# Kernel tuning notes

Hardware: AMD Instinct MI355X
Metric: run time of the kernel (lower is better)

The kernel has to match this reference:

```python
import math
import jax, jax.numpy as jnp
import numpy as np

B, L, D_M, H, D_K, D_V = 2, 2048, 1024, 16, 64, 64


def setup_inputs() -> dict:
    key = jax.random.key(0)
    ks = jax.random.split(key, 12)
    s_in = 1.0 / math.sqrt(D_M)
    s_cat = 1.0 / math.sqrt(H * D_V)
    return {
        "Q": jax.random.normal(ks[0], (B, L, D_M), jnp.float32),
        "K": jax.random.normal(ks[1], (B, L, D_M), jnp.float32),
        "V": jax.random.normal(ks[2], (B, L, D_M), jnp.float32),
        # per-head projections batched along a leading head axis
        "Wq": jax.random.uniform(ks[3], (H, D_M, D_K), jnp.float32, -s_in, s_in),
        "bq": jax.random.uniform(ks[4], (H, D_K), jnp.float32, -s_in, s_in),
        "Wk": jax.random.uniform(ks[5], (H, D_M, D_K), jnp.float32, -s_in, s_in),
        "bk": jax.random.uniform(ks[6], (H, D_K), jnp.float32, -s_in, s_in),
        "Wv": jax.random.uniform(ks[7], (H, D_M, D_V), jnp.float32, -s_in, s_in),
        "bv": jax.random.uniform(ks[8], (H, D_V), jnp.float32, -s_in, s_in),
        "Wo": jax.random.uniform(ks[9], (H * D_V, D_M), jnp.float32, -s_cat, s_cat),
        "bo": jax.random.uniform(ks[10], (D_M,), jnp.float32, -s_cat, s_cat),
    }


def reference(Q, K, V, Wq, bq, Wk, bk, Wv, bv, Wo, bo):
    # Batched per-head projections: [B,L,Dm] x [H,Dm,Dk] -> [B,H,L,Dk]
    Qp = jnp.einsum("bqm,hmk->bhqk", Q, Wq) + bq[None, :, None, :]
    Kp = jnp.einsum("bsm,hmk->bhsk", K, Wk) + bk[None, :, None, :]
    Vp = jnp.einsum("bsm,hmv->bhsv", V, Wv) + bv[None, :, None, :]
    scores = jnp.einsum("bhqk,bhsk->bhqs", Qp, Kp) / jnp.sqrt(
        jnp.asarray(D_K, Qp.dtype)
    )
    # NOTE: original torch code uses Softmax(dim=1) on a [B,Lq,Lk] matrix,
    # i.e. normalization over the QUERY axis (axis=2 here), not the key axis.
    attn = jax.nn.softmax(scores, axis=2)
    wV = jnp.einsum("bhqs,bhsv->bhqv", attn, Vp)  # [B,H,Lq,Dv]
    cat_V = jnp.transpose(wV, (0, 2, 1, 3)).reshape(B, L, H * D_V)
    return cat_V @ Wo + bo
```

## Files before the change

### kernel.cpp

```cpp
#include <hip/hip_runtime.h>
#include <hip/hip_bf16.h>

#define DEVI __device__ __forceinline__

typedef __hip_bfloat16 bf16;
typedef __attribute__((ext_vector_type(8))) __bf16 bf16x8;
typedef __attribute__((ext_vector_type(4))) float f32x4;
typedef __attribute__((ext_vector_type(4))) short short4v;
typedef __attribute__((ext_vector_type(8))) short short8v;


DEVI short bfbits(float f) { bf16 h = __float2bfloat16(f); return *(short*)&h; }
DEVI float b2f(short s) { union { float f; unsigned u; } c; c.u = ((unsigned)(unsigned short)s) << 16; return c.f; }

DEVI void gl16(const void* g, void* l) {
  __builtin_amdgcn_global_load_lds((const __attribute__((address_space(1))) void*)g,
                                   (__attribute__((address_space(3))) void*)l, 16, 0, 0);
}

DEVI f32x4 MF(bf16x8 a, bf16x8 b, f32x4 c) {
  return __builtin_amdgcn_mfma_f32_16x16x32_bf16(a, b, c, 0, 0, 0);
}

DEVI int swzE(int row, int ec) { return row * 64 + (ec ^ ((row & 7) << 3)); }
DEVI int srcC(int boff) { return (boff & 127) ^ (((boff >> 7) & 7) << 4); }

__global__ __launch_bounds__(256) void k_cvt_qkv(
    const float* __restrict__ Q, const float* __restrict__ K, const float* __restrict__ V,
    bf16* __restrict__ Qb, bf16* __restrict__ Kb, bf16* __restrict__ Vb) {
  const float* s = blockIdx.y == 0 ? Q : (blockIdx.y == 1 ? K : V);
  bf16* d = blockIdx.y == 0 ? Qb : (blockIdx.y == 1 ? Kb : Vb);
  int i = (blockIdx.x * 256 + threadIdx.x) * 4;
  float4 v = *(const float4*)(s + i);
  short4v o;
  o[0] = bfbits(v.x); o[1] = bfbits(v.y); o[2] = bfbits(v.z); o[3] = bfbits(v.w);
  *(short4v*)(d + i) = o;
}

__global__ __launch_bounds__(256) void k_prep_w(
    const float* __restrict__ Wq, const float* __restrict__ Wk, const float* __restrict__ Wv,
    const float* __restrict__ Wo,
    bf16* __restrict__ WqT, bf16* __restrict__ WkT, bf16* __restrict__ WvT,
    bf16* __restrict__ WoT) {
  __shared__ float t[64][65];
  const int z = blockIdx.z;
  const float* in; bf16* out; int ldin, ldout;
  if (z < 3) {
    const float* W = z == 0 ? Wq : (z == 1 ? Wk : Wv);
    bf16* O = z == 0 ? WqT : (z == 1 ? WkT : WvT);
    const int hh = blockIdx.y, m0 = blockIdx.x * 64;
    in = W + hh * 65536 + m0 * 64; ldin = 64;
    out = O + hh * 65536 + m0;     ldout = 1024;
  } else {
    const int r0 = blockIdx.x * 64, c0 = blockIdx.y * 64;
    in = Wo + r0 * 1024 + c0; ldin = 1024;
    out = WoT + c0 * 1024 + r0; ldout = 1024;
  }
  const int tx = threadIdx.x & 63, ty = threadIdx.x >> 6;
  for (int r = ty; r < 64; r += 4) t[r][tx] = in[r * ldin + tx];
  __syncthreads();
  for (int c = ty; c < 64; c += 4) out[c * ldout + tx] = __float2bfloat16(t[tx][c]);
}

__global__ __launch_bounds__(256) void k_proj_gemm(
    const bf16* __restrict__ Qb, const bf16* __restrict__ Kb, const bf16* __restrict__ Vb,
    const bf16* __restrict__ WqT, const bf16* __restrict__ WkT, const bf16* __restrict__ WvT,
    const float* __restrict__ bq, const float* __restrict__ bk, const float* __restrict__ bv,
    bf16* __restrict__ Qp, bf16* __restrict__ Kp, bf16* __restrict__ VpT) {
  __shared__ bf16 smem[17408];
  bf16* As = smem;
  bf16* Bs = smem + 8192;
  const int z = blockIdx.z;
  const bf16* A  = z == 0 ? Qb : (z == 1 ? Kb : Vb);
  const bf16* BT = z == 0 ? WqT : (z == 1 ? WkT : WvT);
  const float* bias = z == 0 ? bq : (z == 1 ? bk : bv);
  const int row0 = blockIdx.x * 128, col0 = blockIdx.y * 128;
  const int tid = threadIdx.x, lane = tid & 63, wave = tid >> 6;
  const int wq = wave >> 1, wn = wave & 1;
  f32x4 acc[4][4];
#pragma unroll
  for (int i = 0; i < 4; ++i)
#pragma unroll
    for (int j = 0; j < 4; ++j) acc[i][j] = (f32x4)0.0f;

  for (int k0 = 0; k0 < 1024; k0 += 64) {
#pragma unroll
    for (int it = 0; it < 4; ++it) {
      int boff = (it * 4 + wave) * 1024 + lane * 16;
      int r = boff >> 7, c = srcC(boff);
      gl16((const char*)A  + (size_t)(row0 + r) * 2048 + k0 * 2 + c, (char*)As + boff);
      gl16((const char*)BT + (size_t)(col0 + r) * 2048 + k0 * 2 + c, (char*)Bs + boff);
    }
    __syncthreads();
#pragma unroll
    for (int ks = 0; ks < 2; ++ks) {
      bf16x8 a[4], b[4];
#pragma unroll
      for (int i = 0; i < 4; ++i)
        a[i] = *(const bf16x8*)&As[swzE(wq * 64 + i * 16 + (lane & 15), ks * 32 + (lane >> 4) * 8)];
#pragma unroll
      for (int j = 0; j < 4; ++j)
        b[j] = *(const bf16x8*)&Bs[swzE(wn * 64 + j * 16 + (lane & 15), ks * 32 + (lane >> 4) * 8)];
#pragma unroll
      for (int i = 0; i < 4; ++i)
#pragma unroll
        for (int j = 0; j < 4; ++j) acc[i][j] = MF(a[i], b[j], acc[i][j]);
    }
    __syncthreads();
  }

  if (z < 2) {
    const float scl = (z == 0) ? 0.125f : 1.0f;
    bf16* C = z == 0 ? Qp : Kp;
#pragma unroll
    for (int i = 0; i < 4; ++i)
#pragma unroll
      for (int j = 0; j < 4; ++j) {
        int col = col0 + wn * 64 + j * 16 + (lane & 15);
        float bb = bias[col];
#pragma unroll
        for (int r = 0; r < 4; ++r) {
          int row = row0 + wq * 64 + i * 16 + (lane >> 4) * 4 + r;
          C[row * 1024 + col] = __float2bfloat16((acc[i][j][r] + bb) * scl);
        }
      }
  } else {
    bf16* T = smem;
#pragma unroll
    for (int i = 0; i < 4; ++i)
#pragma unroll
      for (int j = 0; j < 4; ++j) {
        int nl = wn * 64 + j * 16 + (lane & 15);
        float bb = bias[col0 + nl];
#pragma unroll
        for (int r = 0; r < 4; ++r) {
          int sl = wq * 64 + i * 16 + (lane >> 4) * 4 + r;
          T[nl * 136 + sl] = __float2bfloat16(acc[i][j][r] + bb);
        }
      }
    __syncthreads();
    const int b = row0 >> 11, lr = row0 & 2047;
    const int nl = tid >> 1, half = tid & 1;
    const int n = col0 + nl;
    bf16* drow = VpT + ((size_t)(b * 16 + (n >> 6)) * 64 + (n & 63)) * 2048 + lr + half * 64;
#pragma unroll
    for (int k = 0; k < 8; ++k)
      *(short8v*)(drow + k * 8) = *(const short8v*)&T[nl * 136 + half * 64 + k * 8];
  }
}

__global__ __launch_bounds__(512, 4) void k_stats(
    const bf16* __restrict__ Qp, const bf16* __restrict__ Kp, bf16* __restrict__ VpT) {
  __shared__ bf16 Ks[128 * 64];
  __shared__ bf16 Qs[2][64 * 64];
  __shared__ float zs[128];
  const int id = blockIdx.x;
  const int sw = (id & 7) * 64 + (id >> 3);
  const int bh = sw >> 4, s0 = (sw & 15) * 128;
  const int b = bh >> 4, h = bh & 15;
  const char* Qrow = (const char*)(Qp + (size_t)(b * 2048) * 1024 + h * 64);
  const char* Krow = (const char*)(Kp + (size_t)(b * 2048) * 1024 + h * 64);
  const int tid = threadIdx.x, lane = tid & 63, wave = tid >> 6;

  {
    int boff = tid * 16;
#pragma unroll
    for (int it = 0; it < 2; ++it) {
      int bo = boff + it * 8192;
      gl16(Krow + (size_t)(s0 + (bo >> 7)) * 2048 + srcC(bo), (char*)Ks + bo);
    }
    gl16(Qrow + (size_t)(boff >> 7) * 2048 + srcC(boff), (char*)Qs[0] + boff);
  }
  __syncthreads();
  bf16x8 afr[2];
#pragma unroll
  for (int ks = 0; ks < 2; ++ks)
    afr[ks] = *(const bf16x8*)&Ks[swzE(wave * 16 + (lane & 15), ks * 32 + (lane >> 4) * 8)];

  float zr[4] = {0.f, 0.f, 0.f, 0.f};
  for (int c = 0; c < 32; ++c) {
    const int p = c & 1;
    if (c < 31) {
      int boff = tid * 16;
      gl16(Qrow + (size_t)((c + 1) * 64 + (boff >> 7)) * 2048 + srcC(boff), (char*)Qs[p ^ 1] + boff);
    }
    f32x4 acc[4];
#pragma unroll
    for (int qf = 0; qf < 4; ++qf) acc[qf] = (f32x4)0.0f;
#pragma unroll
    for (int ks = 0; ks < 2; ++ks) {
      bf16x8 bfr[4];
#pragma unroll
      for (int qf = 0; qf < 4; ++qf)
        bfr[qf] = *(const bf16x8*)&Qs[p][swzE(qf * 16 + (lane & 15), ks * 32 + (lane >> 4) * 8)];
#pragma unroll
      for (int qf = 0; qf < 4; ++qf) acc[qf] = MF(afr[ks], bfr[qf], acc[qf]);
    }
#pragma unroll
    for (int qf = 0; qf < 4; ++qf)
#pragma unroll
      for (int r = 0; r < 4; ++r) zr[r] += __expf(acc[qf][r]);
    __syncthreads();
  }
#pragma unroll
  for (int m = 1; m <= 8; m <<= 1)
#pragma unroll
    for (int r = 0; r < 4; ++r) zr[r] += __shfl_xor(zr[r], m);
  if ((lane & 15) == 0) {
#pragma unroll
    for (int r = 0; r < 4; ++r) zs[wave * 16 + (lane >> 4) * 4 + r] = 1.0f / zr[r];
  }
  __syncthreads();
  {
    const int v = tid >> 3, seg = tid & 7;
    bf16* base = VpT + (size_t)(bh * 64 + v) * 2048 + s0 + seg * 16;
    short8v x0 = *(const short8v*)base;
    short8v x1 = *(const short8v*)(base + 8);
    short8v o0, o1;
#pragma unroll
    for (int j = 0; j < 8; ++j) {
      o0[j] = bfbits(b2f(x0[j]) * zs[seg * 16 + j]);
      o1[j] = bfbits(b2f(x1[j]) * zs[seg * 16 + 8 + j]);
    }
    *(short8v*)base = o0;
    *(short8v*)(base + 8) = o1;
  }
}

__global__ __launch_bounds__(512, 4) void k_attn_pv(
    const bf16* __restrict__ Qp, const bf16* __restrict__ Kp, const bf16* __restrict__ VpT,
    bf16* __restrict__ wV) {
  __shared__ bf16 QPs[128 * 64];
  __shared__ bf16 Ks[2][64 * 64];
  __shared__ bf16 Vs[2][64 * 64];
  const int id = blockIdx.x;
  const int sw = (id & 7) * 64 + (id >> 3);
  const int bh = sw >> 4, q0 = (sw & 15) * 128;
  const int b = bh >> 4, h = bh & 15;
  const char* Qrow = (const char*)(Qp + (size_t)(b * 2048) * 1024 + h * 64);
  const char* Krow = (const char*)(Kp + (size_t)(b * 2048) * 1024 + h * 64);
  const char* Vrow = (const char*)(VpT + (size_t)bh * 64 * 2048);
  const int tid = threadIdx.x, lane = tid & 63, wave = tid >> 6;

  {
    int boff = tid * 16;
#pragma unroll
    for (int it = 0; it < 2; ++it) {
      int bo = boff + it * 8192;
      gl16(Qrow + (size_t)(q0 + (bo >> 7)) * 2048 + srcC(bo), (char*)QPs + bo);
    }
    gl16(Krow + (size_t)(boff >> 7) * 2048 + srcC(boff), (char*)Ks[0] + boff);
    gl16(Vrow + (size_t)(boff >> 7) * 4096 + srcC(boff), (char*)Vs[0] + boff);
  }
  __syncthreads();
  bf16x8 aq[2];
#pragma unroll
  for (int ks = 0; ks < 2; ++ks)
    aq[ks] = *(const bf16x8*)&QPs[swzE(wave * 16 + (lane & 15), ks * 32 + (lane >> 4) * 8)];

  f32x4 acco[4];
#pragma unroll
  for (int vf = 0; vf < 4; ++vf) acco[vf] = (f32x4)0.0f;

  for (int c = 0; c < 32; ++c) {
    const int p = c & 1;
    if (c < 31) {
      int boff = tid * 16;
      gl16(Krow + (size_t)((c + 1) * 64 + (boff >> 7)) * 2048 + srcC(boff), (char*)Ks[p ^ 1] + boff);
      gl16(Vrow + (size_t)(boff >> 7) * 4096 + (c + 1) * 128 + srcC(boff), (char*)Vs[p ^ 1] + boff);
    }
    f32x4 sacc[4];
#pragma unroll
    for (int sf = 0; sf < 4; ++sf) sacc[sf] = (f32x4)0.0f;
#pragma unroll
    for (int ks = 0; ks < 2; ++ks) {
      bf16x8 bk_[4];
#pragma unroll
      for (int sf = 0; sf < 4; ++sf)
        bk_[sf] = *(const bf16x8*)&Ks[p][swzE(sf * 16 + (lane & 15), ks * 32 + (lane >> 4) * 8)];
#pragma unroll
      for (int sf = 0; sf < 4; ++sf) sacc[sf] = MF(aq[ks], bk_[sf], sacc[sf]);
    }
#pragma unroll
    for (int sf = 0; sf < 4; ++sf) {
      int sl = sf * 16 + (lane & 15);
#pragma unroll
      for (int r = 0; r < 4; ++r) {
        int row = wave * 16 + (lane >> 4) * 4 + r;
        QPs[swzE(row, sl)] = __float2bfloat16(__expf(sacc[sf][r]));
      }
    }
#pragma unroll
    for (int ks = 0; ks < 2; ++ks) {
      bf16x8 pa = *(const bf16x8*)&QPs[swzE(wave * 16 + (lane & 15), ks * 32 + (lane >> 4) * 8)];
      bf16x8 pb[4];
#pragma unroll
      for (int vf = 0; vf < 4; ++vf)
        pb[vf] = *(const bf16x8*)&Vs[p][swzE(vf * 16 + (lane & 15), ks * 32 + (lane >> 4) * 8)];
#pragma unroll
      for (int vf = 0; vf < 4; ++vf) acco[vf] = MF(pa, pb[vf], acco[vf]);
    }
    __syncthreads();
  }

#pragma unroll
  for (int vf = 0; vf < 4; ++vf) {
    int v = vf * 16 + (lane & 15);
#pragma unroll
    for (int r = 0; r < 4; ++r)
      QPs[swzE(wave * 16 + (lane >> 4) * 4 + r, v)] = __float2bfloat16(acco[vf][r]);
  }
  {
    const int rr = wave * 16 + (lane >> 2);
    const int x = (rr & 7) << 3;
    short8v x0 = *(const short8v*)&QPs[rr * 64 + (((lane & 3) * 16) ^ x)];
    short8v x1 = *(const short8v*)&QPs[rr * 64 + (((lane & 3) * 16 + 8) ^ x)];
    bf16* dst = wV + ((size_t)bh * 2048 + q0 + rr) * 64 + (lane & 3) * 16;
    *(short8v*)dst = x0;
    *(short8v*)(dst + 8) = x1;
  }
}

__global__ __launch_bounds__(256) void k_out_gemm(
    const bf16* __restrict__ wV, const bf16* __restrict__ WoT, const float* __restrict__ bo,
    float* __restrict__ out) {
  __shared__ bf16 As[128 * 64], Bs[128 * 64];
  const int row0 = blockIdx.x * 128, col0 = blockIdx.y * 128;
  const int tid = threadIdx.x, lane = tid & 63, wave = tid >> 6;
  const int wq = wave >> 1, wn = wave & 1;
  const int b = row0 >> 11, lr = row0 & 2047;
  f32x4 acc[4][4];
#pragma unroll
  for (int i = 0; i < 4; ++i)
#pragma unroll
    for (int j = 0; j < 4; ++j) acc[i][j] = (f32x4)0.0f;

  for (int k0 = 0; k0 < 1024; k0 += 64) {
    const char* Abase = (const char*)(wV + ((size_t)(b * 16 + (k0 >> 6)) * 2048 + lr) * 64);
#pragma unroll
    for (int it = 0; it < 4; ++it) {
      int boff = (it * 4 + wave) * 1024 + lane * 16;
      int r = boff >> 7, c = srcC(boff);
      gl16(Abase + (size_t)r * 128 + c, (char*)As + boff);
      gl16((const char*)WoT + (size_t)(col0 + r) * 2048 + k0 * 2 + c, (char*)Bs + boff);
    }
    __syncthreads();
#pragma unroll
    for (int ks = 0; ks < 2; ++ks) {
      bf16x8 a[4], bb[4];
#pragma unroll
      for (int i = 0; i < 4; ++i)
        a[i] = *(const bf16x8*)&As[swzE(wq * 64 + i * 16 + (lane & 15), ks * 32 + (lane >> 4) * 8)];
#pragma unroll
      for (int j = 0; j < 4; ++j)
        bb[j] = *(const bf16x8*)&Bs[swzE(wn * 64 + j * 16 + (lane & 15), ks * 32 + (lane >> 4) * 8)];
#pragma unroll
      for (int i = 0; i < 4; ++i)
#pragma unroll
        for (int j = 0; j < 4; ++j) acc[i][j] = MF(a[i], bb[j], acc[i][j]);
    }
    __syncthreads();
  }
#pragma unroll
  for (int i = 0; i < 4; ++i)
#pragma unroll
    for (int j = 0; j < 4; ++j) {
      int col = col0 + wn * 64 + j * 16 + (lane & 15);
      float bb = bo[col];
#pragma unroll
      for (int r = 0; r < 4; ++r) {
        int row = row0 + wq * 64 + i * 16 + (lane >> 4) * 4 + r;
        out[row * 1024 + col] = acc[i][j][r] + bb;
      }
    }
}

extern "C" void kernel_launch(void* const* d_in, const int* in_sizes, int n_in,
                              void* d_out, int out_size, void* d_ws, size_t ws_size,
                              hipStream_t stream) {
  (void)in_sizes; (void)n_in; (void)out_size; (void)ws_size;
  const float* Q  = (const float*)d_in[0];
  const float* K  = (const float*)d_in[1];
  const float* V  = (const float*)d_in[2];
  const float* Wq = (const float*)d_in[3];
  const float* bq = (const float*)d_in[4];
  const float* Wk = (const float*)d_in[5];
  const float* bk = (const float*)d_in[6];
  const float* Wv = (const float*)d_in[7];
  const float* bv = (const float*)d_in[8];
  const float* Wo = (const float*)d_in[9];
  const float* bo = (const float*)d_in[10];

  char* ws = (char*)d_ws;
  bf16* Qb  = (bf16*)(ws);
  bf16* Kb  = (bf16*)(ws + (8u  << 20));
  bf16* Vb  = (bf16*)(ws + (16u << 20));
  bf16* WqT = (bf16*)(ws + (24u << 20));
  bf16* WkT = (bf16*)(ws + (26u << 20));
  bf16* WvT = (bf16*)(ws + (28u << 20));
  bf16* WoT = (bf16*)(ws + (30u << 20));
  bf16* Qp  = (bf16*)(ws + (32u << 20));
  bf16* Kp  = (bf16*)(ws + (40u << 20));
  bf16* VpT = (bf16*)(ws + (48u << 20));
  bf16* wVn = (bf16*)(ws + (56u << 20));

  k_cvt_qkv <<<dim3(4096, 3), 256, 0, stream>>>(Q, K, V, Qb, Kb, Vb);
  k_prep_w  <<<dim3(16, 16, 4), 256, 0, stream>>>(Wq, Wk, Wv, Wo, WqT, WkT, WvT, WoT);
  k_proj_gemm<<<dim3(32, 8, 3), 256, 0, stream>>>(Qb, Kb, Vb, WqT, WkT, WvT, bq, bk, bv, Qp, Kp, VpT);
  k_stats   <<<512, 512, 0, stream>>>(Qp, Kp, VpT);
  k_attn_pv <<<512, 512, 0, stream>>>(Qp, Kp, VpT, wVn);
  k_out_gemm<<<dim3(32, 8), 256, 0, stream>>>(wVn, WoT, bo, (float*)d_out);
}
```

Measured before the change: 262.5 us.

## Switch attention kernels to 32x32x16 MFMA with register-resident P via permlane swap

The stats and attention-PV kernels move from 16x16x32 to 32x32x16 bf16 MFMA, with 4 waves of 32 rows each instead of 8 waves of 16 rows. In k_attn_pv the exp'd score tile is packed to bf16 with v_cvt_pk and rearranged with v_permlane32_swap, so it feeds the PV MFMA straight from registers instead of round-tripping through LDS. The output is also written directly from registers. This cuts LDS traffic and the number of MFMA instructions, at the cost of more registers per thread and fewer threads per block.

```diff
diff --git a/kernel.cpp b/kernel.cpp
--- a/kernel.cpp
+++ b/kernel.cpp
@@ -6,6 +6,7 @@
 typedef __hip_bfloat16 bf16;
 typedef __attribute__((ext_vector_type(8))) __bf16 bf16x8;
 typedef __attribute__((ext_vector_type(4))) float f32x4;
+typedef __attribute__((ext_vector_type(16))) float f32x16;
 typedef __attribute__((ext_vector_type(4))) short short4v;
 typedef __attribute__((ext_vector_type(8))) short short8v;
 
@@ -20,6 +21,23 @@
 
 DEVI f32x4 MF(bf16x8 a, bf16x8 b, f32x4 c) {
   return __builtin_amdgcn_mfma_f32_16x16x32_bf16(a, b, c, 0, 0, 0);
+}
+DEVI f32x16 MF32(bf16x8 a, bf16x8 b, f32x16 c) {
+  return __builtin_amdgcn_mfma_f32_32x32x16_bf16(a, b, c, 0, 0, 0);
+}
+
+DEVI unsigned cvtpk(float lo, float hi) {
+  unsigned w;
+  asm("v_cvt_pk_bf16_f32 %0, %1, %2" : "=v"(w) : "v"(lo), "v"(hi));
+  return w;
+}
+DEVI void swap32(unsigned& a, unsigned& b) {
+  asm volatile("v_permlane32_swap_b32 %0, %1" : "+v"(a), "+v"(b));
+}
+DEVI bf16x8 packB(unsigned w0, unsigned w1, unsigned w2, unsigned w3) {
+  union { unsigned u[4]; bf16x8 v; } t;
+  t.u[0] = w0; t.u[1] = w1; t.u[2] = w2; t.u[3] = w3;
+  return t.v;
 }
 
 DEVI int swzE(int row, int ec) { return row * 64 + (ec ^ ((row & 7) << 3)); }
@@ -149,9 +167,9 @@
   }
 }
 
-__global__ __launch_bounds__(512, 4) void k_stats(
+__global__ __launch_bounds__(256, 2) void k_stats(
     const bf16* __restrict__ Qp, const bf16* __restrict__ Kp, bf16* __restrict__ VpT) {
-  __shared__ bf16 Ks[128 * 64];
+  __shared__ bf16 Kband[128 * 64];
   __shared__ bf16 Qs[2][64 * 64];
   __shared__ float zs[128];
   const int id = blockIdx.x;
@@ -160,77 +178,77 @@
   const int b = bh >> 4, h = bh & 15;
   const char* Qrow = (const char*)(Qp + (size_t)(b * 2048) * 1024 + h * 64);
   const char* Krow = (const char*)(Kp + (size_t)(b * 2048) * 1024 + h * 64);
-  const int tid = threadIdx.x, lane = tid & 63, wave = tid >> 6;
+  const int tid = threadIdx.x, lane = tid & 63, wq = tid >> 6;
+  const int ln31 = lane & 31, hf = lane >> 5;
 
   {
     int boff = tid * 16;
 #pragma unroll
-    for (int it = 0; it < 2; ++it) {
-      int bo = boff + it * 8192;
-      gl16(Krow + (size_t)(s0 + (bo >> 7)) * 2048 + srcC(bo), (char*)Ks + bo);
+    for (int it = 0; it < 4; ++it) {
+      int bo = boff + it * 4096;
+      gl16(Krow + (size_t)(s0 + (bo >> 7)) * 2048 + srcC(bo), (char*)Kband + bo);
     }
     gl16(Qrow + (size_t)(boff >> 7) * 2048 + srcC(boff), (char*)Qs[0] + boff);
+    gl16(Qrow + (size_t)((boff + 4096) >> 7) * 2048 + srcC(boff + 4096), (char*)Qs[0] + boff + 4096);
   }
   __syncthreads();
-  bf16x8 afr[2];
-#pragma unroll
-  for (int ks = 0; ks < 2; ++ks)
-    afr[ks] = *(const bf16x8*)&Ks[swzE(wave * 16 + (lane & 15), ks * 32 + (lane >> 4) * 8)];
-
-  float zr[4] = {0.f, 0.f, 0.f, 0.f};
+  bf16x8 kf[4];
+#pragma unroll
+  for (int ks = 0; ks < 4; ++ks)
+    kf[ks] = *(const bf16x8*)&Kband[swzE(wq * 32 + ln31, ks * 16 + hf * 8)];
+
+  float zp[16];
+#pragma unroll
+  for (int r = 0; r < 16; ++r) zp[r] = 0.f;
+
   for (int c = 0; c < 32; ++c) {
     const int p = c & 1;
     if (c < 31) {
       int boff = tid * 16;
       gl16(Qrow + (size_t)((c + 1) * 64 + (boff >> 7)) * 2048 + srcC(boff), (char*)Qs[p ^ 1] + boff);
-    }
-    f32x4 acc[4];
-#pragma unroll
-    for (int qf = 0; qf < 4; ++qf) acc[qf] = (f32x4)0.0f;
-#pragma unroll
-    for (int ks = 0; ks < 2; ++ks) {
-      bf16x8 bfr[4];
-#pragma unroll
-      for (int qf = 0; qf < 4; ++qf)
-        bfr[qf] = *(const bf16x8*)&Qs[p][swzE(qf * 16 + (lane & 15), ks * 32 + (lane >> 4) * 8)];
-#pragma unroll
-      for (int qf = 0; qf < 4; ++qf) acc[qf] = MF(afr[ks], bfr[qf], acc[qf]);
-    }
-#pragma unroll
-    for (int qf = 0; qf < 4; ++qf)
-#pragma unroll
-      for (int r = 0; r < 4; ++r) zr[r] += __expf(acc[qf][r]);
-    __syncthreads();
-  }
-#pragma unroll
-  for (int m = 1; m <= 8; m <<= 1)
-#pragma unroll
-    for (int r = 0; r < 4; ++r) zr[r] += __shfl_xor(zr[r], m);
-  if ((lane & 15) == 0) {
-#pragma unroll
-    for (int r = 0; r < 4; ++r) zs[wave * 16 + (lane >> 4) * 4 + r] = 1.0f / zr[r];
+      gl16(Qrow + (size_t)((c + 1) * 64 + ((boff + 4096) >> 7)) * 2048 + srcC(boff + 4096),
+           (char*)Qs[p ^ 1] + boff + 4096);
+    }
+    f32x16 sacc0 = (f32x16)0.0f, sacc1 = (f32x16)0.0f;
+#pragma unroll
+    for (int ks = 0; ks < 4; ++ks) {
+      bf16x8 qf0 = *(const bf16x8*)&Qs[p][swzE(ln31, ks * 16 + hf * 8)];
+      bf16x8 qf1 = *(const bf16x8*)&Qs[p][swzE(32 + ln31, ks * 16 + hf * 8)];
+      sacc0 = MF32(kf[ks], qf0, sacc0);
+      sacc1 = MF32(kf[ks], qf1, sacc1);
+    }
+#pragma unroll
+    for (int r = 0; r < 16; ++r) zp[r] += __expf(sacc0[r]) + __expf(sacc1[r]);
+    __syncthreads();
+  }
+#pragma unroll
+  for (int m = 1; m <= 16; m <<= 1)
+#pragma unroll
+    for (int r = 0; r < 16; ++r) zp[r] += __shfl_xor(zp[r], m);
+  if (ln31 == 0) {
+#pragma unroll
+    for (int r = 0; r < 16; ++r)
+      zs[wq * 32 + (r & 3) + 8 * (r >> 2) + 4 * hf] = 1.0f / zp[r];
   }
   __syncthreads();
   {
-    const int v = tid >> 3, seg = tid & 7;
-    bf16* base = VpT + (size_t)(bh * 64 + v) * 2048 + s0 + seg * 16;
-    short8v x0 = *(const short8v*)base;
-    short8v x1 = *(const short8v*)(base + 8);
-    short8v o0, o1;
-#pragma unroll
-    for (int j = 0; j < 8; ++j) {
-      o0[j] = bfbits(b2f(x0[j]) * zs[seg * 16 + j]);
-      o1[j] = bfbits(b2f(x1[j]) * zs[seg * 16 + 8 + j]);
-    }
-    *(short8v*)base = o0;
-    *(short8v*)(base + 8) = o1;
-  }
-}
-
-__global__ __launch_bounds__(512, 4) void k_attn_pv(
+    const int v = tid >> 2, sseg = (tid & 3) * 32;
+    bf16* base = VpT + (size_t)(bh * 64 + v) * 2048 + s0 + sseg;
+#pragma unroll
+    for (int t = 0; t < 4; ++t) {
+      short8v x = *(const short8v*)(base + t * 8);
+      short8v o;
+#pragma unroll
+      for (int j = 0; j < 8; ++j) o[j] = bfbits(b2f(x[j]) * zs[sseg + t * 8 + j]);
+      *(short8v*)(base + t * 8) = o;
+    }
+  }
+}
+
+__global__ __launch_bounds__(256, 2) void k_attn_pv(
     const bf16* __restrict__ Qp, const bf16* __restrict__ Kp, const bf16* __restrict__ VpT,
     bf16* __restrict__ wV) {
-  __shared__ bf16 QPs[128 * 64];
+  __shared__ bf16 Qs[128 * 64];
   __shared__ bf16 Ks[2][64 * 64];
   __shared__ bf16 Vs[2][64 * 64];
   const int id = blockIdx.x;
@@ -240,84 +258,91 @@
   const char* Qrow = (const char*)(Qp + (size_t)(b * 2048) * 1024 + h * 64);
   const char* Krow = (const char*)(Kp + (size_t)(b * 2048) * 1024 + h * 64);
   const char* Vrow = (const char*)(VpT + (size_t)bh * 64 * 2048);
-  const int tid = threadIdx.x, lane = tid & 63, wave = tid >> 6;
+  const int tid = threadIdx.x, lane = tid & 63, wq = tid >> 6;
+  const int ln31 = lane & 31, hf = lane >> 5;
 
   {
     int boff = tid * 16;
 #pragma unroll
+    for (int it = 0; it < 4; ++it) {
+      int bo = boff + it * 4096;
+      gl16(Qrow + (size_t)(q0 + (bo >> 7)) * 2048 + srcC(bo), (char*)Qs + bo);
+    }
+#pragma unroll
     for (int it = 0; it < 2; ++it) {
-      int bo = boff + it * 8192;
-      gl16(Qrow + (size_t)(q0 + (bo >> 7)) * 2048 + srcC(bo), (char*)QPs + bo);
-    }
-    gl16(Krow + (size_t)(boff >> 7) * 2048 + srcC(boff), (char*)Ks[0] + boff);
-    gl16(Vrow + (size_t)(boff >> 7) * 4096 + srcC(boff), (char*)Vs[0] + boff);
+      int bo = boff + it * 4096;
+      gl16(Krow + (size_t)(bo >> 7) * 2048 + srcC(bo), (char*)Ks[0] + bo);
+      gl16(Vrow + (size_t)(bo >> 7) * 4096 + srcC(bo), (char*)Vs[0] + bo);
+    }
   }
   __syncthreads();
-  bf16x8 aq[2];
-#pragma unroll
-  for (int ks = 0; ks < 2; ++ks)
-    aq[ks] = *(const bf16x8*)&QPs[swzE(wave * 16 + (lane & 15), ks * 32 + (lane >> 4) * 8)];
-
-  f32x4 acco[4];
-#pragma unroll
-  for (int vf = 0; vf < 4; ++vf) acco[vf] = (f32x4)0.0f;
+  bf16x8 qf[4];
+#pragma unroll
+  for (int ks = 0; ks < 4; ++ks)
+    qf[ks] = *(const bf16x8*)&Qs[swzE(wq * 32 + ln31, ks * 16 + hf * 8)];
+
+  f32x16 oacc0 = (f32x16)0.0f, oacc1 = (f32x16)0.0f;
 
   for (int c = 0; c < 32; ++c) {
     const int p = c & 1;
     if (c < 31) {
       int boff = tid * 16;
-      gl16(Krow + (size_t)((c + 1) * 64 + (boff >> 7)) * 2048 + srcC(boff), (char*)Ks[p ^ 1] + boff);
-      gl16(Vrow + (size_t)(boff >> 7) * 4096 + (c + 1) * 128 + srcC(boff), (char*)Vs[p ^ 1] + boff);
-    }
-    f32x4 sacc[4];
-#pragma unroll
-    for (int sf = 0; sf < 4; ++sf) sacc[sf] = (f32x4)0.0f;
-#pragma unroll
-    for (int ks = 0; ks < 2; ++ks) {
-      bf16x8 bk_[4];
-#pragma unroll
-      for (int sf = 0; sf < 4; ++sf)
-        bk_[sf] = *(const bf16x8*)&Ks[p][swzE(sf * 16 + (lane & 15), ks * 32 + (lane >> 4) * 8)];
-#pragma unroll
-      for (int sf = 0; sf < 4; ++sf) sacc[sf] = MF(aq[ks], bk_[sf], sacc[sf]);
-    }
-#pragma unroll
-    for (int sf = 0; sf < 4; ++sf) {
-      int sl = sf * 16 + (lane & 15);
-#pragma unroll
-      for (int r = 0; r < 4; ++r) {
-        int row = wave * 16 + (lane >> 4) * 4 + r;
-        QPs[swzE(row, sl)] = __float2bfloat16(__expf(sacc[sf][r]));
-      }
-    }
-#pragma unroll
-    for (int ks = 0; ks < 2; ++ks) {
-      bf16x8 pa = *(const bf16x8*)&QPs[swzE(wave * 16 + (lane & 15), ks * 32 + (lane >> 4) * 8)];
-      bf16x8 pb[4];
-#pragma unroll
-      for (int vf = 0; vf < 4; ++vf)
-        pb[vf] = *(const bf16x8*)&Vs[p][swzE(vf * 16 + (lane & 15), ks * 32 + (lane >> 4) * 8)];
-#pragma unroll
-      for (int vf = 0; vf < 4; ++vf) acco[vf] = MF(pa, pb[vf], acco[vf]);
-    }
-    __syncthreads();
-  }
-
-#pragma unroll
-  for (int vf = 0; vf < 4; ++vf) {
-    int v = vf * 16 + (lane & 15);
-#pragma unroll
-    for (int r = 0; r < 4; ++r)
-      QPs[swzE(wave * 16 + (lane >> 4) * 4 + r, v)] = __float2bfloat16(acco[vf][r]);
-  }
+#pragma unroll
+      for (int it = 0; it < 2; ++it) {
+        int bo = boff + it * 4096;
+        gl16(Krow + (size_t)((c + 1) * 64 + (bo >> 7)) * 2048 + srcC(bo), (char*)Ks[p ^ 1] + bo);
+        gl16(Vrow + (size_t)(bo >> 7) * 4096 + (c + 1) * 128 + srcC(bo), (char*)Vs[p ^ 1] + bo);
+      }
+    }
+    f32x16 sacc0 = (f32x16)0.0f, sacc1 = (f32x16)0.0f;
+#pragma unroll
+    for (int ks = 0; ks < 4; ++ks) {
+      bf16x8 kf0 = *(const bf16x8*)&Ks[p][swzE(ln31, ks * 16 + hf * 8)];
+      bf16x8 kf1 = *(const bf16x8*)&Ks[p][swzE(32 + ln31, ks * 16 + hf * 8)];
+      sacc0 = MF32(kf0, qf[ks], sacc0);
+      sacc1 = MF32(kf1, qf[ks], sacc1);
+    }
+    bf16x8 bfr[4];
+#pragma unroll
+    for (int sb = 0; sb < 2; ++sb) {
+      const f32x16& sa = sb ? sacc1 : sacc0;
+      float pz[16];
+#pragma unroll
+      for (int r = 0; r < 16; ++r) pz[r] = __expf(sa[r]);
+#pragma unroll
+      for (int half = 0; half < 2; ++half) {
+        unsigned w0 = cvtpk(pz[half * 8 + 0], pz[half * 8 + 1]);
+        unsigned w2 = cvtpk(pz[half * 8 + 4], pz[half * 8 + 5]);
+        unsigned w1 = cvtpk(pz[half * 8 + 2], pz[half * 8 + 3]);
+        unsigned w3 = cvtpk(pz[half * 8 + 6], pz[half * 8 + 7]);
+        swap32(w0, w2);
+        swap32(w1, w3);
+        bfr[sb * 2 + half] = packB(w0, w1, w2, w3);
+      }
+    }
+#pragma unroll
+    for (int ks = 0; ks < 4; ++ks) {
+      bf16x8 vf0 = *(const bf16x8*)&Vs[p][swzE(ln31, ks * 16 + hf * 8)];
+      bf16x8 vf1 = *(const bf16x8*)&Vs[p][swzE(32 + ln31, ks * 16 + hf * 8)];
+      oacc0 = MF32(vf0, bfr[ks], oacc0);
+      oacc1 = MF32(vf1, bfr[ks], oacc1);
+    }
+    __syncthreads();
+  }
+
   {
-    const int rr = wave * 16 + (lane >> 2);
-    const int x = (rr & 7) << 3;
-    short8v x0 = *(const short8v*)&QPs[rr * 64 + (((lane & 3) * 16) ^ x)];
-    short8v x1 = *(const short8v*)&QPs[rr * 64 + (((lane & 3) * 16 + 8) ^ x)];
-    bf16* dst = wV + ((size_t)bh * 2048 + q0 + rr) * 64 + (lane & 3) * 16;
-    *(short8v*)dst = x0;
-    *(short8v*)(dst + 8) = x1;
+    char* row = (char*)(wV + ((size_t)bh * 2048 + q0 + wq * 32 + ln31) * 64);
+#pragma unroll
+    for (int vb = 0; vb < 2; ++vb) {
+      const f32x16& oa = vb ? oacc1 : oacc0;
+#pragma unroll
+      for (int qd = 0; qd < 4; ++qd) {
+        uint2 w;
+        w.x = cvtpk(oa[qd * 4 + 0], oa[qd * 4 + 1]);
+        w.y = cvtpk(oa[qd * 4 + 2], oa[qd * 4 + 3]);
+        *(uint2*)(row + vb * 64 + qd * 16 + hf * 8) = w;
+      }
+    }
   }
 }
 
@@ -407,7 +432,7 @@
   k_cvt_qkv <<<dim3(4096, 3), 256, 0, stream>>>(Q, K, V, Qb, Kb, Vb);
   k_prep_w  <<<dim3(16, 16, 4), 256, 0, stream>>>(Wq, Wk, Wv, Wo, WqT, WkT, WvT, WoT);
   k_proj_gemm<<<dim3(32, 8, 3), 256, 0, stream>>>(Qb, Kb, Vb, WqT, WkT, WvT, bq, bk, bv, Qp, Kp, VpT);
-  k_stats   <<<512, 512, 0, stream>>>(Qp, Kp, VpT);
-  k_attn_pv <<<512, 512, 0, stream>>>(Qp, Kp, VpT, wVn);
+  k_stats   <<<512, 256, 0, stream>>>(Qp, Kp, VpT);
+  k_attn_pv <<<512, 256, 0, stream>>>(Qp, Kp, VpT, wVn);
   k_out_gemm<<<dim3(32, 8), 256, 0, stream>>>(wVn, WoT, bo, (float*)d_out);
 }
```

Result: no change. 261.5 us (-0.4%).
